# Kernel optimization log

Measured on AMD Instinct MI355X. Metric: run time of the kernel, lower is better.

Reference implementation:

```python
import jax, jax.numpy as jnp
import numpy as np

EPS = 1e-3

def layer_norm(x, w, b):
    mu = jnp.mean(x, axis=-1, keepdims=True)
    var = jnp.var(x, axis=-1, keepdims=True)
    return (x - mu) * jax.lax.rsqrt(var + EPS) * w + b

def setup_inputs() -> dict:
    key = jax.random.key(0)
    B, T, C, H = 8, 1024, 1024, 16
    Dh, F = C // H, 4 * C
    ks = jax.random.split(key, 12)
    s = 0.02
    return {
        "x":  jax.random.normal(ks[0], (B, T, C), jnp.float32),
        "Wq": jax.random.normal(ks[1], (H, C, Dh), jnp.float32) * s,
        "bq": jnp.zeros((H, Dh), jnp.float32),
        "Wk": jax.random.normal(ks[2], (H, C, Dh), jnp.float32) * s,
        "bk": jnp.zeros((H, Dh), jnp.float32),
        "Wv": jax.random.normal(ks[3], (H, C, Dh), jnp.float32) * s,
        "bv": jnp.zeros((H, Dh), jnp.float32),
        "Wp": jax.random.normal(ks[4], (C, C), jnp.float32) * s,
        "bp": jnp.zeros((C,), jnp.float32),
        "W1": jax.random.normal(ks[5], (C, F), jnp.float32) * s,
        "b1": jnp.zeros((F,), jnp.float32),
        "W2": jax.random.normal(ks[6], (F, C), jnp.float32) * s,
        "b2": jnp.zeros((C,), jnp.float32),
        "ln1_w": jnp.ones((C,), jnp.float32),
        "ln1_b": jnp.zeros((C,), jnp.float32),
        "ln2_w": jnp.ones((C,), jnp.float32),
        "ln2_b": jnp.zeros((C,), jnp.float32),
    }

def reference(x, Wq, bq, Wk, bk, Wv, bv, Wp, bp, W1, b1, W2, b2, ln1_w, ln1_b, ln2_w, ln2_b):
    B, T, C = x.shape
    # x = ln1(x); x = x + mha(x)   (residual taken from post-LN x, as in source)
    x1 = layer_norm(x, ln1_w, ln1_b)
    # all heads vectorized: q/k/v are [B, H, T, Dh]
    q = jnp.einsum('btc,hcd->bhtd', x1, Wq) + bq[:, None, :]
    k = jnp.einsum('btc,hcd->bhtd', x1, Wk) + bk[:, None, :]
    v = jnp.einsum('btc,hcd->bhtd', x1, Wv) + bv[:, None, :]
    # NOTE: source scales by full embed dim C (not head_size), and multiplies
    # the UN-softmaxed scores `wei` by v (softmax result is discarded).
    wei = jnp.einsum('bhtd,bhsd->bhts', q, k) * (C ** -0.5)
    heads = jnp.einsum('bhts,bhsd->bhtd', wei, v)            # [B,H,T,Dh]
    cat = heads.transpose(0, 2, 1, 3).reshape(B, T, C)        # concat heads
    attn = cat @ Wp + bp
    x2 = layer_norm(x1 + attn, ln2_w, ln2_b)
    h = jax.nn.gelu(x2 @ W1 + b1, approximate=False)
    return x2 + (h @ W2 + b2)
```

## Files before the change

kernel.cpp:

```cpp
#include <hip/hip_runtime.h>

typedef unsigned short u16;
typedef unsigned int u32;
typedef unsigned long long u64;
typedef __attribute__((ext_vector_type(8))) short bf16x8;
typedef __attribute__((ext_vector_type(4))) float f32x4;

__device__ __forceinline__ float b2f(u16 v) {
  union { u32 u; float f; } c; c.u = ((u32)v) << 16; return c.f;
}
__device__ __forceinline__ u16 f2b(float f) {
  union { float f; u32 u; } c; c.f = f;
  return (u16)((c.u + 0x7fffu + ((c.u >> 16) & 1u)) >> 16);
}

__device__ __forceinline__ void g2l16(const u16* g, u16* l) {
  __builtin_amdgcn_global_load_lds(
      (const __attribute__((address_space(1))) u32*)g,
      (__attribute__((address_space(3))) u32*)l,
      16, 0, 0);
}

__device__ __forceinline__ float gelu_fast(float x) {
  float z2 = -1.5957691216057308f * x * (1.0f + 0.044715f * x * x);
  z2 = fminf(fmaxf(z2, -30.f), 30.f);
  float t = __expf(z2);
  return x * __builtin_amdgcn_rcpf(1.0f + t);
}

__global__ __launch_bounds__(256)
void repack_qkv_tiled(const float* __restrict__ Wq, const float* __restrict__ Wk,
                      const float* __restrict__ Wv, u16* __restrict__ WT) {
  __shared__ u16 tile[64][65];
  const int sh = blockIdx.y, sel = sh >> 4, h = sh & 15;
  const float* W = (sel == 0) ? Wq : ((sel == 1) ? Wk : Wv);
  const int k0 = blockIdx.x * 64;
  {
    const int d = threadIdx.x & 63, r = threadIdx.x >> 6;
    #pragma unroll
    for (int i = 0; i < 16; ++i) {
      int k = r * 16 + i;
      tile[k][d] = f2b(W[(size_t)h * 65536 + (size_t)(k0 + k) * 64 + d]);
    }
  }
  __syncthreads();
  {
    const int k = threadIdx.x & 63, dd = threadIdx.x >> 6;
    #pragma unroll
    for (int i = 0; i < 16; ++i) {
      int d2 = dd * 16 + i;
      WT[((size_t)sel * 1024 + h * 64 + d2) * 1024 + k0 + k] = tile[k][d2];
    }
  }
}

__global__ __launch_bounds__(256)
void transpose_tiled(const float* __restrict__ W, u16* __restrict__ WT,
                     int N, int K) {
  __shared__ u16 tile[32][33];
  const int bx = blockIdx.x * 32;
  const int by = blockIdx.y * 32;
  const int tx = threadIdx.x & 31, ty = threadIdx.x >> 5;
  #pragma unroll
  for (int i = 0; i < 4; ++i) {
    int k = ty + i * 8;
    tile[k][tx] = f2b(W[(size_t)(by + k) * N + bx + tx]);
  }
  __syncthreads();
  #pragma unroll
  for (int i = 0; i < 4; ++i) {
    int n = ty + i * 8;
    WT[(size_t)(bx + n) * K + by + tx] = tile[tx][n];
  }
}

__global__ __launch_bounds__(256)
void ln_f32_kernel(const float* __restrict__ X, const float* __restrict__ G,
                   const float* __restrict__ Bt, u16* __restrict__ O) {
  const int row = blockIdx.x;
  const int tid = threadIdx.x;
  const float* xr = X + (size_t)row * 1024;
  float4 xv = *(const float4*)(xr + tid * 4);
  float v0 = xv.x, v1 = xv.y, v2 = xv.z, v3 = xv.w;
  float s = v0 + v1 + v2 + v3;
  float q = v0 * v0 + v1 * v1 + v2 * v2 + v3 * v3;
  #pragma unroll
  for (int off = 32; off > 0; off >>= 1) {
    s += __shfl_down(s, off);
    q += __shfl_down(q, off);
  }
  __shared__ float red[8];
  int wave = tid >> 6, lane = tid & 63;
  if (lane == 0) { red[wave] = s; red[4 + wave] = q; }
  __syncthreads();
  s = red[0] + red[1] + red[2] + red[3];
  q = red[4] + red[5] + red[6] + red[7];
  float mean = s * (1.f / 1024.f);
  float var = q * (1.f / 1024.f) - mean * mean;
  float rstd = rsqrtf(var + 1e-3f);
  float4 gv = *(const float4*)(G + tid * 4);
  float4 bv = *(const float4*)(Bt + tid * 4);
  ushort4 ov;
  ov.x = f2b((v0 - mean) * rstd * gv.x + bv.x);
  ov.y = f2b((v1 - mean) * rstd * gv.y + bv.y);
  ov.z = f2b((v2 - mean) * rstd * gv.z + bv.z);
  ov.w = f2b((v3 - mean) * rstd * gv.w + bv.w);
  *(ushort4*)(O + (size_t)row * 1024 + tid * 4) = ov;
}

__global__ __launch_bounds__(256)
void ln_bf16_kernel(const u16* __restrict__ X, const float* __restrict__ G,
                    const float* __restrict__ Bt, u16* __restrict__ O) {
  const int row = blockIdx.x;
  const int tid = threadIdx.x;
  const u16* xr = X + (size_t)row * 1024;
  ushort4 xv = *(const ushort4*)(xr + tid * 4);
  float v0 = b2f(xv.x), v1 = b2f(xv.y), v2 = b2f(xv.z), v3 = b2f(xv.w);
  float s = v0 + v1 + v2 + v3;
  float q = v0 * v0 + v1 * v1 + v2 * v2 + v3 * v3;
  #pragma unroll
  for (int off = 32; off > 0; off >>= 1) {
    s += __shfl_down(s, off);
    q += __shfl_down(q, off);
  }
  __shared__ float red[8];
  int wave = tid >> 6, lane = tid & 63;
  if (lane == 0) { red[wave] = s; red[4 + wave] = q; }
  __syncthreads();
  s = red[0] + red[1] + red[2] + red[3];
  q = red[4] + red[5] + red[6] + red[7];
  float mean = s * (1.f / 1024.f);
  float var = q * (1.f / 1024.f) - mean * mean;
  float rstd = rsqrtf(var + 1e-3f);
  float4 gv = *(const float4*)(G + tid * 4);
  float4 bv = *(const float4*)(Bt + tid * 4);
  ushort4 ov;
  ov.x = f2b((v0 - mean) * rstd * gv.x + bv.x);
  ov.y = f2b((v1 - mean) * rstd * gv.y + bv.y);
  ov.z = f2b((v2 - mean) * rstd * gv.z + bv.z);
  ov.w = f2b((v3 - mean) * rstd * gv.w + bv.w);
  *(ushort4*)(O + (size_t)row * 1024 + tid * 4) = ov;
}

template <int EPI>
__global__ __launch_bounds__(256)
void gemm_nt(const u16* __restrict__ A, const u16* __restrict__ BT,
             void* __restrict__ Cout,
             const float* __restrict__ bias0, const float* __restrict__ bias1,
             const float* __restrict__ bias2, const u16* __restrict__ resid,
             int M, int N, int K) {
  __shared__ __align__(16) u16 smem[16384];
  u16* As = smem;
  u16* Bs = smem + 8192;
  const int tid = threadIdx.x;

  const u32 nb = gridDim.x;
  u32 bid = blockIdx.x;
  bid = (bid & 7) * (nb >> 3) + (bid >> 3);
  const u32 gx = (u32)N >> 7;
  const int m0 = (int)(bid / gx) * 128;
  const int n0 = (int)(bid % gx) * 128;

  const int wave = tid >> 6, lane = tid & 63;
  const int wm = wave & 1, wn = wave >> 1;
  const int quad = lane >> 4, l16 = lane & 15;

  f32x4 acc[4][4];
  #pragma unroll
  for (int i = 0; i < 4; ++i)
    #pragma unroll
    for (int j = 0; j < 4; ++j) acc[i][j] = (f32x4){0.f, 0.f, 0.f, 0.f};

  const int rowS = tid >> 3;
  const int swz = ((tid & 7) ^ ((tid >> 3) & 7)) * 8;
  const u16* aB = A + (size_t)(m0 + rowS) * K + swz;
  const u16* bB = BT + (size_t)(n0 + rowS) * K + swz;
  u16* aD = &As[(u32)tid * 8];
  u16* bD = &Bs[(u32)tid * 8];
  const size_t rstep = (size_t)32 * K;

  for (int k0 = 0; k0 < K; k0 += 64) {
    #pragma unroll
    for (int cc = 0; cc < 4; ++cc) {
      g2l16(aB + k0 + cc * rstep, aD + cc * 2048);
      g2l16(bB + k0 + cc * rstep, bD + cc * 2048);
    }
    __syncthreads();
    #pragma unroll
    for (int ks = 0; ks < 2; ++ks) {
      const int sOff = (((ks * 4 + quad) ^ (l16 & 7)) * 8);
      bf16x8 aF[4], bF[4];
      #pragma unroll
      for (int i = 0; i < 4; ++i)
        aF[i] = *(const bf16x8*)&As[(wm * 64 + i * 16 + l16) * 64 + sOff];
      #pragma unroll
      for (int j = 0; j < 4; ++j)
        bF[j] = *(const bf16x8*)&Bs[(wn * 64 + j * 16 + l16) * 64 + sOff];
      #pragma unroll
      for (int i = 0; i < 4; ++i)
        #pragma unroll
        for (int j = 0; j < 4; ++j)
          acc[i][j] = __builtin_amdgcn_mfma_f32_16x16x32_bf16(aF[i], bF[j], acc[i][j], 0, 0, 0);
    }
    __syncthreads();
  }

  #pragma unroll
  for (int half = 0; half < 2; ++half) {
    if (wm == half) {
      #pragma unroll
      for (int i = 0; i < 4; ++i) {
        const int fsw = (i * 4 + quad) & 7;
        #pragma unroll
        for (int j = 0; j < 4; ++j) {
          const int chunk = (wn * 8 + j * 2 + (l16 >> 3)) ^ fsw;
          const int base = chunk * 8 + (l16 & 7);
          #pragma unroll
          for (int rr = 0; rr < 4; ++rr) {
            const int lrow = i * 16 + quad * 4 + rr;
            smem[lrow * 128 + base] = f2b(acc[i][j][rr]);
          }
        }
      }
    }
    __syncthreads();
    #pragma unroll
    for (int s = 0; s < 4; ++s) {
      const int lrow = s * 16 + (tid >> 4);
      const int chunk = tid & 15;
      const int fsw = (lrow >> 2) & 7;
      bf16x8 cv = *(const bf16x8*)&smem[lrow * 128 + ((chunk ^ fsw) * 8)];
      const int gr = m0 + half * 64 + lrow;
      const int gc = n0 + chunk * 8;
      const float* bp_ = bias0;
      int cb = gc;
      if (EPI == 0) {
        const int selb = gc >> 10;
        bp_ = (selb == 0) ? bias0 : ((selb == 1) ? bias1 : bias2);
        cb = gc & 1023;
      }
      float4 bv0 = *(const float4*)(bp_ + cb);
      float4 bv1 = *(const float4*)(bp_ + cb + 4);
      float vv[8];
      #pragma unroll
      for (int e = 0; e < 8; ++e) {
        float be = (e < 4) ? ((const float*)&bv0)[e] : ((const float*)&bv1)[e - 4];
        vv[e] = b2f(((const u16*)&cv)[e]) + be;
      }
      if (EPI == 2) {
        #pragma unroll
        for (int e = 0; e < 8; ++e) vv[e] = gelu_fast(vv[e]);
      }
      if (EPI == 1 || EPI == 3) {
        bf16x8 rv = *(const bf16x8*)(resid + (size_t)gr * N + gc);
        #pragma unroll
        for (int e = 0; e < 8; ++e) vv[e] += b2f(((const u16*)&rv)[e]);
      }
      if (EPI == 3) {
        float4 o0 = {vv[0], vv[1], vv[2], vv[3]};
        float4 o1 = {vv[4], vv[5], vv[6], vv[7]};
        float* op = (float*)Cout + (size_t)gr * N + gc;
        *(float4*)op = o0;
        *(float4*)(op + 4) = o1;
      } else {
        bf16x8 ov;
        #pragma unroll
        for (int e = 0; e < 8; ++e) ((u16*)&ov)[e] = f2b(vv[e]);
        *(bf16x8*)((u16*)Cout + (size_t)gr * N + gc) = ov;
      }
    }
    __syncthreads();
  }
}

__global__ __launch_bounds__(256)
void attn_m_kernel(const u16* __restrict__ qkv, float* __restrict__ Mbuf) {
  const int bh = blockIdx.x;
  const int half = blockIdx.y;
  const int b = bh >> 4, h = bh & 15;
  const u16* Kp = qkv + (size_t)b * 1024 * 3072 + 1024 + h * 64;
  const u16* Vp = Kp + 1024 + half * 32;
  __shared__ __align__(16) float Ks[64 * 64];
  __shared__ __align__(16) float Vs[64 * 36];
  const int tid = threadIdx.x;
  const int d1 = tid & 63, d2b = (tid >> 6) * 8;
  const int lr = tid >> 3, lc = (tid & 7) * 8;
  const int vr = tid >> 2, vc = (tid & 3) * 8;
  float acc[8];
  #pragma unroll
  for (int j = 0; j < 8; ++j) acc[j] = 0.f;
  for (int t0 = 0; t0 < 1024; t0 += 64) {
    __syncthreads();
    #pragma unroll
    for (int it = 0; it < 2; ++it) {
      int r = it * 32 + lr;
      const u16* ks = Kp + (size_t)(t0 + r) * 3072 + lc;
      ushort4 a0 = *(const ushort4*)ks;
      ushort4 a1 = *(const ushort4*)(ks + 4);
      float* kd = &Ks[r * 64 + lc];
      kd[0] = b2f(a0.x); kd[1] = b2f(a0.y); kd[2] = b2f(a0.z); kd[3] = b2f(a0.w);
      kd[4] = b2f(a1.x); kd[5] = b2f(a1.y); kd[6] = b2f(a1.z); kd[7] = b2f(a1.w);
    }
    {
      const u16* vs = Vp + (size_t)(t0 + vr) * 3072 + vc;
      ushort4 c0 = *(const ushort4*)vs;
      ushort4 c1 = *(const ushort4*)(vs + 4);
      float* vd = &Vs[vr * 36 + vc];
      vd[0] = b2f(c0.x); vd[1] = b2f(c0.y); vd[2] = b2f(c0.z); vd[3] = b2f(c0.w);
      vd[4] = b2f(c1.x); vd[5] = b2f(c1.y); vd[6] = b2f(c1.z); vd[7] = b2f(c1.w);
    }
    __syncthreads();
    #pragma unroll 8
    for (int tt = 0; tt < 64; ++tt) {
      float kv = Ks[tt * 64 + d1];
      #pragma unroll
      for (int j = 0; j < 8; ++j) acc[j] += kv * Vs[tt * 36 + d2b + j];
    }
  }
  float* Mo = Mbuf + (size_t)bh * 4096 + d1 * 64 + half * 32 + d2b;
  #pragma unroll
  for (int j = 0; j < 8; ++j) Mo[j] = acc[j] * 0.03125f;
}

__global__ __launch_bounds__(256)
void attn_h_kernel(const u16* __restrict__ qkv, const float* __restrict__ Mbuf,
                   u16* __restrict__ cat) {
  const int bh = blockIdx.x;
  const int tch = blockIdx.y;
  const int b = bh >> 4, h = bh & 15;
  __shared__ __align__(16) float Ms[64 * 64];
  __shared__ __align__(16) float Qs[64 * 65];
  const int tid = threadIdx.x;
  const float* Msrc = Mbuf + (size_t)bh * 4096;
  #pragma unroll
  for (int i = 0; i < 16; ++i) Ms[i * 256 + tid] = Msrc[i * 256 + tid];
  const u16* Qp = qkv + (size_t)(b * 1024 + tch * 64) * 3072 + h * 64;
  {
    const int lr = tid >> 3, lc = (tid & 7) * 8;
    #pragma unroll
    for (int it = 0; it < 2; ++it) {
      int r = it * 32 + lr;
      const u16* qs = Qp + (size_t)r * 3072 + lc;
      ushort4 a0 = *(const ushort4*)qs;
      ushort4 a1 = *(const ushort4*)(qs + 4);
      float* qd = &Qs[r * 65 + lc];
      qd[0] = b2f(a0.x); qd[1] = b2f(a0.y); qd[2] = b2f(a0.z); qd[3] = b2f(a0.w);
      qd[4] = b2f(a1.x); qd[5] = b2f(a1.y); qd[6] = b2f(a1.z); qd[7] = b2f(a1.w);
    }
  }
  __syncthreads();
  const int tl = tid >> 2, db = (tid & 3) * 16;
  float acc[16];
  #pragma unroll
  for (int j = 0; j < 16; ++j) acc[j] = 0.f;
  #pragma unroll 4
  for (int k = 0; k < 64; ++k) {
    float qv = Qs[tl * 65 + k];
    #pragma unroll
    for (int j = 0; j < 16; ++j) acc[j] += qv * Ms[k * 64 + db + j];
  }
  u16* Cp = cat + (size_t)(b * 1024 + tch * 64 + tl) * 1024 + h * 64 + db;
  ushort4 o0 = {f2b(acc[0]), f2b(acc[1]), f2b(acc[2]), f2b(acc[3])};
  ushort4 o1 = {f2b(acc[4]), f2b(acc[5]), f2b(acc[6]), f2b(acc[7])};
  ushort4 o2 = {f2b(acc[8]), f2b(acc[9]), f2b(acc[10]), f2b(acc[11])};
  ushort4 o3 = {f2b(acc[12]), f2b(acc[13]), f2b(acc[14]), f2b(acc[15])};
  *(ushort4*)(Cp + 0) = o0;
  *(ushort4*)(Cp + 4) = o1;
  *(ushort4*)(Cp + 8) = o2;
  *(ushort4*)(Cp + 12) = o3;
}

extern "C" void kernel_launch(void* const* d_in, const int* in_sizes, int n_in,
                              void* d_out, int out_size, void* d_ws, size_t ws_size,
                              hipStream_t stream) {
  (void)in_sizes; (void)n_in; (void)out_size; (void)ws_size;
  const float* x     = (const float*)d_in[0];
  const float* Wq    = (const float*)d_in[1];
  const float* bq    = (const float*)d_in[2];
  const float* Wk    = (const float*)d_in[3];
  const float* bk    = (const float*)d_in[4];
  const float* Wv    = (const float*)d_in[5];
  const float* bv    = (const float*)d_in[6];
  const float* Wp    = (const float*)d_in[7];
  const float* bp    = (const float*)d_in[8];
  const float* W1    = (const float*)d_in[9];
  const float* b1    = (const float*)d_in[10];
  const float* W2    = (const float*)d_in[11];
  const float* b2    = (const float*)d_in[12];
  const float* ln1w  = (const float*)d_in[13];
  const float* ln1b  = (const float*)d_in[14];
  const float* ln2w  = (const float*)d_in[15];
  const float* ln2b  = (const float*)d_in[16];

  char* ws = (char*)d_ws;
  u16* x1    = (u16*)(ws);
  u16* qkv   = (u16*)(ws + 16777216);
  u16* cat   = (u16*)(ws + 67108864);
  u16* yb    = (u16*)(ws + 83886080);
  u16* x2    = (u16*)(ws + 100663296);
  u16* WqkvT = (u16*)(ws + 117440512);
  u16* WpT   = (u16*)(ws + 123731968);
  u16* W1T   = (u16*)(ws + 125829120);
  u16* W2T   = (u16*)(ws + 134217728);
  float* Mb  = (float*)(ws + 142606336);
  u16* hb    = (u16*)(ws + 16777216);

  repack_qkv_tiled<<<dim3(16, 48), 256, 0, stream>>>(Wq, Wk, Wv, WqkvT);
  transpose_tiled<<<dim3(32, 32), 256, 0, stream>>>(Wp, WpT, 1024, 1024);
  transpose_tiled<<<dim3(128, 32), 256, 0, stream>>>(W1, W1T, 4096, 1024);
  transpose_tiled<<<dim3(32, 128), 256, 0, stream>>>(W2, W2T, 1024, 4096);

  ln_f32_kernel<<<8192, 256, 0, stream>>>(x, ln1w, ln1b, x1);

  gemm_nt<0><<<1536, 256, 0, stream>>>(x1, WqkvT, qkv, bq, bk, bv, nullptr,
                                       8192, 3072, 1024);
  attn_m_kernel<<<dim3(128, 2), 256, 0, stream>>>(qkv, Mb);
  attn_h_kernel<<<dim3(128, 16), 256, 0, stream>>>(qkv, Mb, cat);

  gemm_nt<1><<<512, 256, 0, stream>>>(cat, WpT, yb, bp, nullptr, nullptr, x1,
                                      8192, 1024, 1024);
  ln_bf16_kernel<<<8192, 256, 0, stream>>>(yb, ln2w, ln2b, x2);

  gemm_nt<2><<<2048, 256, 0, stream>>>(x2, W1T, hb, b1, nullptr, nullptr, nullptr,
                                       8192, 4096, 1024);
  gemm_nt<3><<<512, 256, 0, stream>>>(hb, W2T, d_out, b2, nullptr, nullptr, x2,
                                      8192, 1024, 4096);
}
```

Measured before the change: 537.1 us.

## Double-buffer GEMM LDS tiles and switch to 2D grid without XCD swizzle

The GEMM now keeps two LDS buffers (64KB) and issues the async global-to-LDS loads for the next K tile right after reading the current tile's fragments. This overlaps memory loads with MFMA work and uses one barrier per iteration instead of two. The block-ID remapping that spread tiles across XCDs is removed in favour of a plain 2D grid, which may change L2 locality. Doubling LDS per block may also lower occupancy.

```diff
diff --git a/kernel.cpp b/kernel.cpp
--- a/kernel.cpp
+++ b/kernel.cpp
@@ -149,18 +149,10 @@
              const float* __restrict__ bias0, const float* __restrict__ bias1,
              const float* __restrict__ bias2, const u16* __restrict__ resid,
              int M, int N, int K) {
-  __shared__ __align__(16) u16 smem[16384];
-  u16* As = smem;
-  u16* Bs = smem + 8192;
+  __shared__ __align__(16) u16 smem[32768];
   const int tid = threadIdx.x;
-
-  const u32 nb = gridDim.x;
-  u32 bid = blockIdx.x;
-  bid = (bid & 7) * (nb >> 3) + (bid >> 3);
-  const u32 gx = (u32)N >> 7;
-  const int m0 = (int)(bid / gx) * 128;
-  const int n0 = (int)(bid % gx) * 128;
-
+  const int m0 = blockIdx.y * 128;
+  const int n0 = blockIdx.x * 128;
   const int wave = tid >> 6, lane = tid & 63;
   const int wm = wave & 1, wn = wave >> 1;
   const int quad = lane >> 4, l16 = lane & 15;
@@ -175,35 +167,52 @@
   const int swz = ((tid & 7) ^ ((tid >> 3) & 7)) * 8;
   const u16* aB = A + (size_t)(m0 + rowS) * K + swz;
   const u16* bB = BT + (size_t)(n0 + rowS) * K + swz;
-  u16* aD = &As[(u32)tid * 8];
-  u16* bD = &Bs[(u32)tid * 8];
   const size_t rstep = (size_t)32 * K;
 
-  for (int k0 = 0; k0 < K; k0 += 64) {
+  const int nt = K >> 6;
+
+  auto stage = [&](int p, int kt) {
+    u16* aD = &smem[(u32)p * 8192 + (u32)tid * 8];
+    u16* bD = &smem[16384u + (u32)p * 8192 + (u32)tid * 8];
+    const int k0 = kt * 64;
     #pragma unroll
     for (int cc = 0; cc < 4; ++cc) {
       g2l16(aB + k0 + cc * rstep, aD + cc * 2048);
       g2l16(bB + k0 + cc * rstep, bD + cc * 2048);
     }
-    __syncthreads();
+  };
+
+  stage(0, 0);
+
+  for (int t = 0; t < nt; ++t) {
+    const int p = t & 1;
+    asm volatile("s_waitcnt vmcnt(0)" ::: "memory");
+    __builtin_amdgcn_s_barrier();
+    const u16* As = &smem[(u32)p * 8192];
+    const u16* Bs = &smem[16384u + (u32)p * 8192];
+
+    bf16x8 aF[2][4], bF[2][4];
     #pragma unroll
     for (int ks = 0; ks < 2; ++ks) {
       const int sOff = (((ks * 4 + quad) ^ (l16 & 7)) * 8);
-      bf16x8 aF[4], bF[4];
       #pragma unroll
       for (int i = 0; i < 4; ++i)
-        aF[i] = *(const bf16x8*)&As[(wm * 64 + i * 16 + l16) * 64 + sOff];
+        aF[ks][i] = *(const bf16x8*)&As[(wm * 64 + i * 16 + l16) * 64 + sOff];
       #pragma unroll
       for (int j = 0; j < 4; ++j)
-        bF[j] = *(const bf16x8*)&Bs[(wn * 64 + j * 16 + l16) * 64 + sOff];
+        bF[ks][j] = *(const bf16x8*)&Bs[(wn * 64 + j * 16 + l16) * 64 + sOff];
+    }
+    if (t + 1 < nt) stage(p ^ 1, t + 1);
+    #pragma unroll
+    for (int ks = 0; ks < 2; ++ks)
       #pragma unroll
       for (int i = 0; i < 4; ++i)
         #pragma unroll
         for (int j = 0; j < 4; ++j)
-          acc[i][j] = __builtin_amdgcn_mfma_f32_16x16x32_bf16(aF[i], bF[j], acc[i][j], 0, 0, 0);
-    }
-    __syncthreads();
-  }
+          acc[i][j] = __builtin_amdgcn_mfma_f32_16x16x32_bf16(
+              aF[ks][i], bF[ks][j], acc[i][j], 0, 0, 0);
+  }
+  __syncthreads();
 
   #pragma unroll
   for (int half = 0; half < 2; ++half) {
@@ -412,17 +421,17 @@
 
   ln_f32_kernel<<<8192, 256, 0, stream>>>(x, ln1w, ln1b, x1);
 
-  gemm_nt<0><<<1536, 256, 0, stream>>>(x1, WqkvT, qkv, bq, bk, bv, nullptr,
-                                       8192, 3072, 1024);
+  gemm_nt<0><<<dim3(24, 64), 256, 0, stream>>>(x1, WqkvT, qkv, bq, bk, bv, nullptr,
+                                               8192, 3072, 1024);
   attn_m_kernel<<<dim3(128, 2), 256, 0, stream>>>(qkv, Mb);
   attn_h_kernel<<<dim3(128, 16), 256, 0, stream>>>(qkv, Mb, cat);
 
-  gemm_nt<1><<<512, 256, 0, stream>>>(cat, WpT, yb, bp, nullptr, nullptr, x1,
-                                      8192, 1024, 1024);
+  gemm_nt<1><<<dim3(8, 64), 256, 0, stream>>>(cat, WpT, yb, bp, nullptr, nullptr, x1,
+                                              8192, 1024, 1024);
   ln_bf16_kernel<<<8192, 256, 0, stream>>>(yb, ln2w, ln2b, x2);
 
-  gemm_nt<2><<<2048, 256, 0, stream>>>(x2, W1T, hb, b1, nullptr, nullptr, nullptr,
-                                       8192, 4096, 1024);
-  gemm_nt<3><<<512, 256, 0, stream>>>(hb, W2T, d_out, b2, nullptr, nullptr, x2,
-                                      8192, 1024, 4096);
-}
+  gemm_nt<2><<<dim3(32, 64), 256, 0, stream>>>(x2, W1T, hb, b1, nullptr, nullptr, nullptr,
+                                               8192, 4096, 1024);
+  gemm_nt<3><<<dim3(8, 64), 256, 0, stream>>>(hb, W2T, d_out, b2, nullptr, nullptr, x2,
+                                              8192, 1024, 4096);
+}
```

Result: faster. 523.4 us (-2.6%).
